# Kernel tuning notes

Measured on AMD Instinct MI355X. Metric: run time of the kernel, lower is better.

Reference implementation:

```python
import jax, jax.numpy as jnp
import numpy as np

B, S, HID = 2, 2048, 4096
NH, NKV, HD = 32, 8, 128
GRP = NH // NKV          # query heads per kv head
G = 128                  # weight quant group size
FP8_MAX = 448.0          # e4m3 max
EPS = 1e-6


def _rmsnorm(x, w):
    return x * jax.lax.rsqrt(jnp.mean(x * x, axis=-1, keepdims=True) + EPS) * w


def _act_quant(x):
    # per-token fp8 quantization: scale = amax/448, values clipped to fp8 range
    s = jnp.max(jnp.abs(x), axis=-1, keepdims=True) / FP8_MAX
    s = jnp.maximum(s, 1e-6)
    return jnp.clip(x / s, -FP8_MAX, FP8_MAX), s


def _deq_weight(wi4, wscale):
    # wi4: [out, in] int values in [0,16) -> signed int4 [-8,7]
    # wscale: [out, in//G] per-group scales, broadcast along input dim
    return (wi4.astype(jnp.float32) - 8.0) * jnp.repeat(wscale, G, axis=1)


def _rotate_half(x):
    x1, x2 = jnp.split(x, 2, axis=-1)
    return jnp.concatenate([-x2, x1], axis=-1)


def setup_inputs() -> dict:
    key = jax.random.key(0)
    ks = jax.random.split(key, 8)
    hidden_states = jax.random.normal(ks[0], (B, S, HID), dtype=jnp.float32)
    ln_weight = jnp.ones((HID,), dtype=jnp.float32)
    # real RoPE tables
    inv_freq = 1.0 / (10000.0 ** (np.arange(0, HD, 2, dtype=np.float32) / HD))
    ang = np.arange(S, dtype=np.float32)[:, None] * inv_freq[None, :]
    emb = np.concatenate([ang, ang], axis=-1)  # [S, HD]
    cos = jnp.broadcast_to(jnp.asarray(np.cos(emb)), (B, S, HD)).astype(jnp.float32)
    sin = jnp.broadcast_to(jnp.asarray(np.sin(emb)), (B, S, HD)).astype(jnp.float32)
    def wq(k, out, inp):
        ki, ksc = jax.random.split(k)
        wi = jax.random.randint(ki, (out, inp), 0, 16, dtype=jnp.int32)
        sc = jax.random.uniform(ksc, (out, inp // G), dtype=jnp.float32) * 0.01 + 0.001
        return wi, sc
    wq_i4, wq_scale = wq(ks[1], NH * HD, HID)
    wk_i4, wk_scale = wq(ks[2], NKV * HD, HID)
    wv_i4, wv_scale = wq(ks[3], NKV * HD, HID)
    wo_i4, wo_scale = wq(ks[4], HID, NH * HD)
    return dict(hidden_states=hidden_states, ln_weight=ln_weight, cos=cos, sin=sin,
                wq_scale=wq_scale, wk_scale=wk_scale, wv_scale=wv_scale, wo_scale=wo_scale,
                wq_i4=wq_i4, wk_i4=wk_i4, wv_i4=wv_i4, wo_i4=wo_i4)


def reference(hidden_states, ln_weight, cos, sin,
              wq_scale, wk_scale, wv_scale, wo_scale,
              wq_i4, wk_i4, wv_i4, wo_i4):
    b, s, _ = hidden_states.shape
    residual = hidden_states
    h = _rmsnorm(hidden_states, ln_weight)
    qx, qx_s = _act_quant(h)                     # [b,s,HID], [b,s,1]
    q = (qx @ _deq_weight(wq_i4, wq_scale).T) * qx_s
    k = (qx @ _deq_weight(wk_i4, wk_scale).T) * qx_s
    v = (qx @ _deq_weight(wv_i4, wv_scale).T) * qx_s
    q = q.reshape(b, s, NH, HD)
    k = k.reshape(b, s, NKV, HD)
    v = v.reshape(b, s, NKV, HD)
    cse, sne = cos[:, :, None, :], sin[:, :, None, :]
    q = q * cse + _rotate_half(q) * sne
    k = k * cse + _rotate_half(k) * sne
    # GQA causal attention (fp8 fmha numerics emulated in fp32)
    qg = q.reshape(b, s, NKV, GRP, HD)
    scaling = HD ** -0.5
    scores = jnp.einsum('bskgd,btkd->bkgst', qg, k) * scaling  # [b,kv,g,s,t]
    causal = jnp.tril(jnp.ones((s, s), dtype=bool))
    scores = jnp.where(causal, scores, jnp.float32(-1e30))
    p = jax.nn.softmax(scores, axis=-1)
    o = jnp.einsum('bkgst,btkd->bskgd', p, v).reshape(b, s, NH * HD)
    qo, qo_s = _act_quant(o)
    out = (qo @ _deq_weight(wo_i4, wo_scale).T) * qo_s + residual
    return out
```

## Files before the change

kernel.cpp:

```cpp
#include <hip/hip_runtime.h>
#include <stdint.h>

#define HID    4096
#define SLEN   2048
#define BATCH  2
#define NHEADS 32
#define NKVH   8
#define HDIM   128
#define NTOK   (BATCH*SLEN)
#define NQK    (NHEADS*HDIM)
#define NKVD   (NKVH*HDIM)
#define NQKV   (NQK + 2*NKVD)
#define ASTR   (NQK + NKVD)

typedef unsigned short u16;
typedef short short8 __attribute__((ext_vector_type(8)));
typedef float f32x4 __attribute__((ext_vector_type(4)));
typedef int int4v __attribute__((ext_vector_type(4)));
typedef u16 u16x4 __attribute__((ext_vector_type(4)));

static __device__ __forceinline__ u16 f2bf(float f) {
  unsigned u = __builtin_bit_cast(unsigned, f);
  u += 0x7FFFu + ((u >> 16) & 1u);
  return (u16)(u >> 16);
}
static __device__ __forceinline__ float bf2f(u16 h) {
  return __builtin_bit_cast(float, (unsigned)h << 16);
}
static __device__ __forceinline__ void gload_lds16(const void* g, void* l) {
  __builtin_amdgcn_global_load_lds((const __attribute__((address_space(1))) void*)g,
                                   (__attribute__((address_space(3))) void*)l, 16, 0, 0);
}

__global__ __launch_bounds__(256) void k_rmsnorm(const float* __restrict__ x,
                                                 const float* __restrict__ w,
                                                 u16* __restrict__ h) {
  const int row = blockIdx.x;
  const float4* xr = (const float4*)(x + (size_t)row * HID);
  float4 vals[4];
  float ss = 0.f;
#pragma unroll
  for (int i = 0; i < 4; ++i) {
    float4 v = xr[threadIdx.x + i * 256];
    vals[i] = v;
    ss += v.x*v.x + v.y*v.y + v.z*v.z + v.w*v.w;
  }
#pragma unroll
  for (int off = 32; off; off >>= 1) ss += __shfl_xor(ss, off);
  __shared__ float red[4];
  if ((threadIdx.x & 63) == 0) red[threadIdx.x >> 6] = ss;
  __syncthreads();
  ss = red[0] + red[1] + red[2] + red[3];
  const float scale = rsqrtf(ss * (1.f / HID) + 1e-6f);
  u16* hr = h + (size_t)row * HID;
#pragma unroll
  for (int i = 0; i < 4; ++i) {
    int c = (threadIdx.x + i * 256) * 4;
    float4 v = vals[i];
    unsigned lo = (unsigned)f2bf(v.x * scale * w[c])   | ((unsigned)f2bf(v.y * scale * w[c+1]) << 16);
    unsigned hi = (unsigned)f2bf(v.z * scale * w[c+2]) | ((unsigned)f2bf(v.w * scale * w[c+3]) << 16);
    *(unsigned long long*)(hr + c) = ((unsigned long long)hi << 32) | lo;
  }
}

__global__ __launch_bounds__(256) void k_deq(const int* __restrict__ W,
                                             const float* __restrict__ Ws,
                                             u16* __restrict__ out) {
  const int idx = blockIdx.x * 256 + threadIdx.x;
  const int n = idx >> 9;
  const int k8 = (idx & 511) * 8;
  const float sc = Ws[n * 32 + (k8 >> 7)];
  int4v a = *(const int4v*)(W + (size_t)n * HID + k8);
  int4v b = *(const int4v*)(W + (size_t)n * HID + k8 + 4);
  u16 r[8];
#pragma unroll
  for (int j = 0; j < 4; ++j) r[j]     = f2bf((float)(a[j] - 8) * sc);
#pragma unroll
  for (int j = 0; j < 4; ++j) r[j + 4] = f2bf((float)(b[j] - 8) * sc);
  *(short8*)(out + (size_t)n * HID + k8) = *(short8*)r;
}

#define KD 4096
#define NT 64

#define STAGE_A_(nb, kt, mh)                                                   \
  { _Pragma("unroll") for (int r_ = 0; r_ < 2; ++r_) {                         \
      const int base_ = (mh)*64 + r_*128 + wave*8;                             \
      const int lr_ = base_ + (lane>>3);                                       \
      gload_lds16(Ag + (size_t)(m0 + lr_)*KD + (kt)*64 + (((lane&7) ^ (lr_&7))<<3), \
                  lA[nb] + base_*64); } }

#define STAGE_B_(nb, kt, nh)                                                   \
  { _Pragma("unroll") for (int r_ = 0; r_ < 2; ++r_) {                         \
      const int w8_ = r_*64 + wave*8;                                          \
      const int base_ = ((w8_>>5)<<6) + (nh)*32 + (w8_&31);                    \
      const int nr_ = base_ + (lane>>3);                                       \
      gload_lds16(Bg + (size_t)(n0 + nr_)*KD + (kt)*64 + (((lane&7) ^ (nr_&7))<<3), \
                  lB[nb] + base_*64); } }

#define DS_PHASE(buf, mh, nh)                                                  \
  { const int kb_ = lane >> 4;                                                 \
    _Pragma("unroll") for (int ks = 0; ks < 2; ++ks) {                         \
      _Pragma("unroll") for (int i = 0; i < 4; ++i) {                          \
        const int lr_ = wm*128 + (mh)*64 + i*16 + (lane & 15);                 \
        af[i][ks] = *(const short8*)(lA[buf] + lr_*64 + (((ks*4+kb_) ^ (lr_&7))<<3)); } \
      _Pragma("unroll") for (int j = 0; j < 2; ++j) {                          \
        const int nr_ = wn*64 + (nh)*32 + j*16 + (lane & 15);                  \
        bf[j][ks] = *(const short8*)(lB[buf] + nr_*64 + (((ks*4+kb_) ^ (nr_&7))<<3)); } } }

#define MFMA_PHASE(mh, nh)                                                     \
  __builtin_amdgcn_s_setprio(1);                                               \
  _Pragma("unroll") for (int ks = 0; ks < 2; ++ks)                             \
    _Pragma("unroll") for (int i = 0; i < 4; ++i)                              \
      _Pragma("unroll") for (int j = 0; j < 2; ++j)                            \
        acc[(mh)*4+i][(nh)*2+j] = __builtin_amdgcn_mfma_f32_16x16x32_bf16(     \
            af[i][ks], bf[j][ks], acc[(mh)*4+i][(nh)*2+j], 0, 0, 0);           \
  __builtin_amdgcn_s_setprio(0);

#define BAR()  __builtin_amdgcn_s_barrier(); asm volatile("" ::: "memory")
#define VMW(n) asm volatile("s_waitcnt vmcnt(" #n ")" ::: "memory")

#define GEMM8P_BODY                                                            \
  __shared__ __align__(16) u16 lA[2][256*64];                                  \
  __shared__ __align__(16) u16 lB[2][256*64];                                  \
  const int tid = threadIdx.x, lane = tid & 63, wave = tid >> 6;               \
  const int wm = wave >> 2, wn = wave & 3;                                     \
  f32x4 acc[8][4];                                                             \
  _Pragma("unroll") for (int mi = 0; mi < 8; ++mi)                             \
    _Pragma("unroll") for (int ni = 0; ni < 4; ++ni)                           \
      acc[mi][ni] = (f32x4){0.f, 0.f, 0.f, 0.f};                               \
  short8 af[4][2], bf[2][2];                                                   \
  STAGE_A_(0, 0, 0); STAGE_B_(0, 0, 0); STAGE_A_(0, 0, 1); STAGE_B_(0, 0, 1);  \
  VMW(4); BAR();                                                               \
  for (int t = 0; t < NT - 1; ++t) {                                           \
    const int cur = t & 1, nxt = cur ^ 1;                                      \
    DS_PHASE(cur, 0, 0);                                                       \
    STAGE_A_(nxt, t + 1, 0);                                                   \
    BAR();                                                                     \
    MFMA_PHASE(0, 0);                                                          \
    VMW(2); BAR();                                                             \
    DS_PHASE(cur, 0, 1);                                                       \
    STAGE_B_(nxt, t + 1, 0);                                                   \
    BAR();                                                                     \
    MFMA_PHASE(0, 1);                                                          \
    BAR();                                                                     \
    DS_PHASE(cur, 1, 0);                                                       \
    STAGE_A_(nxt, t + 1, 1);                                                   \
    BAR();                                                                     \
    MFMA_PHASE(1, 0);                                                          \
    BAR();                                                                     \
    DS_PHASE(cur, 1, 1);                                                       \
    STAGE_B_(nxt, t + 1, 1);                                                   \
    BAR();                                                                     \
    MFMA_PHASE(1, 1);                                                          \
    VMW(4); BAR();                                                             \
  }                                                                            \
  {                                                                            \
    const int cur = (NT - 1) & 1;                                              \
    DS_PHASE(cur, 0, 0);                                                       \
    BAR();                                                                     \
    MFMA_PHASE(0, 0);                                                          \
    VMW(0); BAR();                                                             \
    DS_PHASE(cur, 0, 1);                                                       \
    BAR();                                                                     \
    MFMA_PHASE(0, 1);                                                          \
    BAR();                                                                     \
    DS_PHASE(cur, 1, 0);                                                       \
    BAR();                                                                     \
    MFMA_PHASE(1, 0);                                                          \
    BAR();                                                                     \
    DS_PHASE(cur, 1, 1);                                                       \
    BAR();                                                                     \
    MFMA_PHASE(1, 1);                                                          \
  }

__global__ __launch_bounds__(512, 2) void k_gemm_qkv_8p(
    const u16* __restrict__ Ag, const u16* __restrict__ Bg,
    u16* __restrict__ C, u16* __restrict__ Vt) {
  const int wg = (blockIdx.x & 7) * 48 + (blockIdx.x >> 3);
  const int m0 = (wg & 15) * 256;
  const int n0 = (wg >> 4) * 256;
  GEMM8P_BODY
  if (n0 < ASTR) {
#pragma unroll
    for (int mi = 0; mi < 8; ++mi) {
      const int row = m0 + wm * 128 + mi * 16 + ((lane >> 4) << 2);
#pragma unroll
      for (int ni = 0; ni < 4; ++ni) {
        const int col = n0 + wn * 64 + ni * 16 + (lane & 15);
#pragma unroll
        for (int r = 0; r < 4; ++r)
          C[(size_t)(row + r) * ASTR + col] = f2bf(acc[mi][ni][r]);
      }
    }
  } else {
#pragma unroll
    for (int mi = 0; mi < 8; ++mi) {
      const int row = m0 + wm * 128 + mi * 16 + ((lane >> 4) << 2);
      const int b_ = row >> 11, s_ = row & 2047;
#pragma unroll
      for (int ni = 0; ni < 4; ++ni) {
        const int colv = (n0 - ASTR) + wn * 64 + ni * 16 + (lane & 15);
        u16x4 pk;
#pragma unroll
        for (int r = 0; r < 4; ++r) pk[r] = f2bf(acc[mi][ni][r]);
        *(u16x4*)(Vt + ((size_t)(b_ * NKVH + (colv >> 7)) * HDIM + (colv & 127)) * SLEN + s_) = pk;
      }
    }
  }
}

__global__ __launch_bounds__(512, 2) void k_gemm_o_8p(
    const u16* __restrict__ Ag, const u16* __restrict__ Bg,
    const float* __restrict__ resid, float* __restrict__ out) {
  const int wg = (blockIdx.x & 7) * 32 + (blockIdx.x >> 3);
  const int m0 = (wg & 15) * 256;
  const int n0 = (wg >> 4) * 256;
  GEMM8P_BODY
#pragma unroll
  for (int mi = 0; mi < 8; ++mi) {
    const int row = m0 + wm * 128 + mi * 16 + ((lane >> 4) << 2);
#pragma unroll
    for (int ni = 0; ni < 4; ++ni) {
      const int col = n0 + wn * 64 + ni * 16 + (lane & 15);
#pragma unroll
      for (int r = 0; r < 4; ++r) {
        const size_t idx = (size_t)(row + r) * HID + col;
        out[idx] = acc[mi][ni][r] + resid[idx];
      }
    }
  }
}

#define BM 128
#define BN 128
#define BK 64

__global__ __launch_bounds__(256) void k_gemm_qkv(
    const u16* __restrict__ A,
    const int* __restrict__ Wq, const int* __restrict__ Wk, const int* __restrict__ Wv,
    const float* __restrict__ Sq, const float* __restrict__ Sk, const float* __restrict__ Sv,
    u16* __restrict__ C, u16* __restrict__ Vt) {
  __shared__ __align__(16) u16 lA[BM * BK];
  __shared__ __align__(16) u16 lB[BN * BK];
  const int tid = threadIdx.x;
  const int lane = tid & 63;
  const int wave = tid >> 6;
  const int wm = wave >> 1, wn = wave & 1;
  const int m0 = blockIdx.x * BM;
  const int n0 = blockIdx.y * BN;

  const int* W; const float* Ws; int nb;
  if (n0 < NQK)       { W = Wq; Ws = Sq; nb = n0; }
  else if (n0 < ASTR) { W = Wk; Ws = Sk; nb = n0 - NQK; }
  else                { W = Wv; Ws = Sv; nb = n0 - ASTR; }

  const int mloc = wave * 8 + (lane >> 3);
  const int lb8 = (((lane & 7) ^ (lane >> 3)) << 3);

  f32x4 acc[4][4];
#pragma unroll
  for (int mi = 0; mi < 4; ++mi)
#pragma unroll
    for (int ni = 0; ni < 4; ++ni) acc[mi][ni] = (f32x4){0.f, 0.f, 0.f, 0.f};

  for (int k0 = 0; k0 < HID; k0 += BK) {
    __syncthreads();
#pragma unroll
    for (int p = 0; p < 4; ++p)
      gload_lds16(A + (size_t)(m0 + p * 32 + mloc) * HID + k0 + lb8,
                  lA + p * 2048 + wave * 512);
    const int grp = k0 >> 7;
#pragma unroll
    for (int p = 0; p < 8; ++p) {
      const int n = p * 16 + (tid >> 4);
      const int kk = (tid & 15) * 4;
      int4v wv4 = *(const int4v*)(W + (size_t)(nb + n) * HID + k0 + kk);
      const float sc = Ws[(nb + n) * 32 + grp];
      unsigned lo = (unsigned)f2bf((float)(wv4[0] - 8) * sc) |
                    ((unsigned)f2bf((float)(wv4[1] - 8) * sc) << 16);
      unsigned hi = (unsigned)f2bf((float)(wv4[2] - 8) * sc) |
                    ((unsigned)f2bf((float)(wv4[3] - 8) * sc) << 16);
      const int di = (n * 64 + kk) ^ ((n & 7) << 3);
      unsigned* dst = (unsigned*)(lB + di);
      dst[0] = lo; dst[1] = hi;
    }
    __syncthreads();
#pragma unroll
    for (int kc = 0; kc < 2; ++kc) {
      const int kOff = kc * 32 + ((lane >> 4) << 3);
      short8 af[4], bfr[4];
#pragma unroll
      for (int i = 0; i < 4; ++i) {
        const int m = wm * 64 + i * 16 + (lane & 15);
        af[i] = *(const short8*)(lA + ((m * 64 + kOff) ^ ((m & 7) << 3)));
        const int n = wn * 64 + i * 16 + (lane & 15);
        bfr[i] = *(const short8*)(lB + ((n * 64 + kOff) ^ ((n & 7) << 3)));
      }
#pragma unroll
      for (int mi = 0; mi < 4; ++mi)
#pragma unroll
        for (int ni = 0; ni < 4; ++ni)
          acc[mi][ni] = __builtin_amdgcn_mfma_f32_16x16x32_bf16(af[mi], bfr[ni], acc[mi][ni], 0, 0, 0);
    }
  }
  if (n0 < ASTR) {
#pragma unroll
    for (int mi = 0; mi < 4; ++mi) {
      const int row = m0 + wm * 64 + mi * 16 + ((lane >> 4) << 2);
#pragma unroll
      for (int ni = 0; ni < 4; ++ni) {
        const int col = n0 + wn * 64 + ni * 16 + (lane & 15);
#pragma unroll
        for (int r = 0; r < 4; ++r)
          C[(size_t)(row + r) * ASTR + col] = f2bf(acc[mi][ni][r]);
      }
    }
  } else {
#pragma unroll
    for (int mi = 0; mi < 4; ++mi) {
      const int row = m0 + wm * 64 + mi * 16 + ((lane >> 4) << 2);
      const int b_ = row >> 11, s_ = row & 2047;
#pragma unroll
      for (int ni = 0; ni < 4; ++ni) {
        const int colv = (n0 - ASTR) + wn * 64 + ni * 16 + (lane & 15);
        u16x4 pk;
#pragma unroll
        for (int r = 0; r < 4; ++r) pk[r] = f2bf(acc[mi][ni][r]);
        *(u16x4*)(Vt + ((size_t)(b_ * NKVH + (colv >> 7)) * HDIM + (colv & 127)) * SLEN + s_) = pk;
      }
    }
  }
}

__global__ __launch_bounds__(256) void k_gemm_o(
    const u16* __restrict__ A, const int* __restrict__ W, const float* __restrict__ Ws,
    const float* __restrict__ resid, float* __restrict__ out) {
  __shared__ __align__(16) u16 lA[BM * BK];
  __shared__ __align__(16) u16 lB[BN * BK];
  const int tid = threadIdx.x;
  const int lane = tid & 63;
  const int wave = tid >> 6;
  const int wm = wave >> 1, wn = wave & 1;
  const int m0 = blockIdx.x * BM;
  const int n0 = blockIdx.y * BN;

  const int mloc = wave * 8 + (lane >> 3);
  const int lb8 = (((lane & 7) ^ (lane >> 3)) << 3);

  f32x4 acc[4][4];
#pragma unroll
  for (int mi = 0; mi < 4; ++mi)
#pragma unroll
    for (int ni = 0; ni < 4; ++ni) acc[mi][ni] = (f32x4){0.f, 0.f, 0.f, 0.f};

  for (int k0 = 0; k0 < NQK; k0 += BK) {
    __syncthreads();
#pragma unroll
    for (int p = 0; p < 4; ++p)
      gload_lds16(A + (size_t)(m0 + p * 32 + mloc) * NQK + k0 + lb8,
                  lA + p * 2048 + wave * 512);
    const int grp = k0 >> 7;
#pragma unroll
    for (int p = 0; p < 8; ++p) {
      const int n = p * 16 + (tid >> 4);
      const int kk = (tid & 15) * 4;
      int4v wv4 = *(const int4v*)(W + (size_t)(n0 + n) * NQK + k0 + kk);
      const float sc = Ws[(n0 + n) * 32 + grp];
      unsigned lo = (unsigned)f2bf((float)(wv4[0] - 8) * sc) |
                    ((unsigned)f2bf((float)(wv4[1] - 8) * sc) << 16);
      unsigned hi = (unsigned)f2bf((float)(wv4[2] - 8) * sc) |
                    ((unsigned)f2bf((float)(wv4[3] - 8) * sc) << 16);
      const int di = (n * 64 + kk) ^ ((n & 7) << 3);
      unsigned* dst = (unsigned*)(lB + di);
      dst[0] = lo; dst[1] = hi;
    }
    __syncthreads();
#pragma unroll
    for (int kc = 0; kc < 2; ++kc) {
      const int kOff = kc * 32 + ((lane >> 4) << 3);
      short8 af[4], bfr[4];
#pragma unroll
      for (int i = 0; i < 4; ++i) {
        const int m = wm * 64 + i * 16 + (lane & 15);
        af[i] = *(const short8*)(lA + ((m * 64 + kOff) ^ ((m & 7) << 3)));
        const int n = wn * 64 + i * 16 + (lane & 15);
        bfr[i] = *(const short8*)(lB + ((n * 64 + kOff) ^ ((n & 7) << 3)));
      }
#pragma unroll
      for (int mi = 0; mi < 4; ++mi)
#pragma unroll
        for (int ni = 0; ni < 4; ++ni)
          acc[mi][ni] = __builtin_amdgcn_mfma_f32_16x16x32_bf16(af[mi], bfr[ni], acc[mi][ni], 0, 0, 0);
      }
  }
#pragma unroll
  for (int mi = 0; mi < 4; ++mi) {
    const int row = m0 + wm * 64 + mi * 16 + ((lane >> 4) << 2);
#pragma unroll
    for (int ni = 0; ni < 4; ++ni) {
      const int col = n0 + wn * 64 + ni * 16 + (lane & 15);
#pragma unroll
      for (int r = 0; r < 4; ++r) {
        const size_t idx = (size_t)(row + r) * HID + col;
        out[idx] = acc[mi][ni][r] + resid[idx];
      }
    }
  }
}

__global__ __launch_bounds__(256) void k_rope(u16* __restrict__ qk,
                                              const float* __restrict__ cosb,
                                              const float* __restrict__ sinb) {
  const int idx = blockIdx.x * 256 + threadIdx.x;
  const int d = idx & 63;
  const int hh = (idx >> 6) % 40;
  const int t = idx / (64 * 40);
  const int col = (hh < 32) ? hh * HDIM : NQK + (hh - 32) * HDIM;
  u16* p = qk + (size_t)t * ASTR + col;
  const float c = cosb[t * HDIM + d], s = sinb[t * HDIM + d];
  const float x1 = bf2f(p[d]), x2 = bf2f(p[d + 64]);
  p[d]      = f2bf(x1 * c - x2 * s);
  p[d + 64] = f2bf(x2 * c + x1 * s);
}

__global__ __launch_bounds__(256) void k_attn(const u16* __restrict__ qk,
                                              const u16* __restrict__ vt,
                                              u16* __restrict__ o) {
  const int slot = blockIdx.x;
  const int w = (slot & 7) * 128 + (slot >> 3);
  const int qi = 15 - (w & 15);
  const int h = (w >> 4) & 31;
  const int b = w >> 9;
  const int kvh = h >> 2;
  const int q0 = qi * 128;
  const int lane = threadIdx.x & 63, wave = threadIdx.x >> 6;
  const int m = lane & 15, kg = lane >> 4;

  const u16* Qb = qk + (size_t)b * SLEN * ASTR + h * HDIM;
  const u16* Kb = qk + (size_t)b * SLEN * ASTR + NQK + kvh * HDIM;
  const u16* Vb = vt + (size_t)(b * NKVH + kvh) * HDIM * SLEN;

  __shared__ __align__(16) u16 Kt[64 * 128];
  __shared__ __align__(16) u16 Vts[128 * 64];
  __shared__ __align__(16) u16 Pl[4][32 * 72];

  const int qr = q0 + wave * 32;
  short8 qf[2][4];
#pragma unroll
  for (int mi = 0; mi < 2; ++mi)
#pragma unroll
    for (int kc = 0; kc < 4; ++kc)
      qf[mi][kc] = *(const short8*)(Qb + (size_t)(qr + mi * 16 + m) * ASTR + kc * 32 + kg * 8);

  f32x4 oacc[2][8];
#pragma unroll
  for (int mi = 0; mi < 2; ++mi)
#pragma unroll
    for (int n = 0; n < 8; ++n) oacc[mi][n] = (f32x4){0.f, 0.f, 0.f, 0.f};
  float rm[2][4], rl[2][4];
#pragma unroll
  for (int mi = 0; mi < 2; ++mi)
#pragma unroll
    for (int r = 0; r < 4; ++r) { rm[mi][r] = -3.0e38f; rl[mi][r] = 0.f; }

  const float sscale = 0.08838834764831845f;
  const int nt = q0 / 64 + 2;
  for (int t = 0; t < nt; ++t) {
    const int kv0 = t * 64;
    __syncthreads();
#pragma unroll
    for (int p = 0; p < 4; ++p) {
      const int row = p * 16 + wave * 4 + (lane >> 4);
      const int c8s = (lane & 15) ^ (row & 7);
      gload_lds16(Kb + (size_t)(kv0 + row) * ASTR + c8s * 8, Kt + p * 2048 + wave * 512);
    }
#pragma unroll
    for (int p = 0; p < 4; ++p) {
      const int d = p * 32 + wave * 8 + (lane >> 3);
      const int c8s = (lane & 7) ^ (d & 7);
      gload_lds16(Vb + (size_t)d * SLEN + kv0 + c8s * 8, Vts + p * 2048 + wave * 512);
    }
    __syncthreads();

    f32x4 sf[2][4];
#pragma unroll
    for (int mi = 0; mi < 2; ++mi)
#pragma unroll
      for (int ni = 0; ni < 4; ++ni) sf[mi][ni] = (f32x4){0.f, 0.f, 0.f, 0.f};
#pragma unroll
    for (int ni = 0; ni < 4; ++ni)
#pragma unroll
      for (int kc = 0; kc < 4; ++kc) {
        const int krow = ni * 16 + m;
        short8 kf = *(const short8*)(Kt + krow * 128 + (((kc * 4 + kg) ^ (krow & 7)) << 3));
#pragma unroll
        for (int mi = 0; mi < 2; ++mi)
          sf[mi][ni] = __builtin_amdgcn_mfma_f32_16x16x32_bf16(qf[mi][kc], kf, sf[mi][ni], 0, 0, 0);
      }

#pragma unroll
    for (int mi = 0; mi < 2; ++mi) {
      const bool dg = (kv0 + 63 > qr + mi * 16);
      float tmax[4] = {-3.0e38f, -3.0e38f, -3.0e38f, -3.0e38f};
#pragma unroll
      for (int ni = 0; ni < 4; ++ni)
#pragma unroll
        for (int r = 0; r < 4; ++r) {
          float s = sf[mi][ni][r] * sscale;
          if (dg) {
            const int rowg = qr + mi * 16 + kg * 4 + r;
            const int colg = kv0 + ni * 16 + m;
            if (colg > rowg) s = -1e30f;
          }
          sf[mi][ni][r] = s;
          tmax[r] = fmaxf(tmax[r], s);
        }
#pragma unroll
      for (int r = 0; r < 4; ++r)
#pragma unroll
        for (int off = 1; off < 16; off <<= 1)
          tmax[r] = fmaxf(tmax[r], __shfl_xor(tmax[r], off));
      float scl[4], psum[4];
#pragma unroll
      for (int r = 0; r < 4; ++r) {
        const float mn = fmaxf(rm[mi][r], tmax[r]);
        scl[r] = __expf(rm[mi][r] - mn);
        rm[mi][r] = mn;
        psum[r] = 0.f;
      }
#pragma unroll
      for (int ni = 0; ni < 4; ++ni)
#pragma unroll
        for (int r = 0; r < 4; ++r) {
          const float p = __expf(sf[mi][ni][r] - rm[mi][r]);
          psum[r] += p;
          Pl[wave][(mi * 16 + kg * 4 + r) * 72 + ni * 16 + m] = f2bf(p);
        }
#pragma unroll
      for (int r = 0; r < 4; ++r) {
#pragma unroll
        for (int off = 1; off < 16; off <<= 1)
          psum[r] += __shfl_xor(psum[r], off);
        rl[mi][r] = rl[mi][r] * scl[r] + psum[r];
      }
#pragma unroll
      for (int n = 0; n < 8; ++n)
#pragma unroll
        for (int r = 0; r < 4; ++r) oacc[mi][n][r] *= scl[r];
    }

#pragma unroll
    for (int kc = 0; kc < 2; ++kc) {
      short8 pf[2];
#pragma unroll
      for (int mi = 0; mi < 2; ++mi)
        pf[mi] = *(const short8*)(&Pl[wave][(mi * 16 + m) * 72 + kc * 32 + kg * 8]);
#pragma unroll
      for (int n = 0; n < 8; ++n) {
        const int vrow = n * 16 + m;
        short8 vf = *(const short8*)(Vts + vrow * 64 + (((kc * 4 + kg) ^ (vrow & 7)) << 3));
#pragma unroll
        for (int mi = 0; mi < 2; ++mi)
          oacc[mi][n] = __builtin_amdgcn_mfma_f32_16x16x32_bf16(pf[mi], vf, oacc[mi][n], 0, 0, 0);
      }
    }
  }

#pragma unroll
  for (int mi = 0; mi < 2; ++mi) {
    float inv[4];
#pragma unroll
    for (int r = 0; r < 4; ++r) inv[r] = 1.0f / rl[mi][r];
#pragma unroll
    for (int n = 0; n < 8; ++n)
#pragma unroll
      for (int r = 0; r < 4; ++r) {
        const int row = qr + mi * 16 + kg * 4 + r;
        o[((size_t)b * SLEN + row) * NQK + h * HDIM + n * 16 + m] = f2bf(oacc[mi][n][r] * inv[r]);
      }
  }
}

extern "C" void kernel_launch(void* const* d_in, const int* in_sizes, int n_in,
                              void* d_out, int out_size, void* d_ws, size_t ws_size,
                              hipStream_t stream) {
  (void)in_sizes; (void)n_in; (void)out_size;
  const float* x    = (const float*)d_in[0];
  const float* lnw  = (const float*)d_in[1];
  const float* cosb = (const float*)d_in[2];
  const float* sinb = (const float*)d_in[3];
  const float* sq   = (const float*)d_in[4];
  const float* sk   = (const float*)d_in[5];
  const float* sv   = (const float*)d_in[6];
  const float* so   = (const float*)d_in[7];
  const int* wq     = (const int*)d_in[8];
  const int* wk     = (const int*)d_in[9];
  const int* wv     = (const int*)d_in[10];
  const int* wo     = (const int*)d_in[11];

  u16* h   = (u16*)d_ws;
  u16* qkb = h + (size_t)NTOK * HID;
  u16* vtb = qkb + (size_t)NTOK * ASTR;
  u16* wqkvb = vtb + (size_t)BATCH * NKVH * HDIM * SLEN;
  u16* wob   = wqkvb + (size_t)NQKV * HID;
  float* out = (float*)d_out;

  const size_t need = ((size_t)NTOK * HID + (size_t)NTOK * ASTR +
                       (size_t)BATCH * NKVH * HDIM * SLEN +
                       (size_t)NQKV * HID + (size_t)HID * NQK) * sizeof(u16);
  const bool predeq = (ws_size >= need);

  k_rmsnorm<<<NTOK, 256, 0, stream>>>(x, lnw, h);

  if (predeq) {
    k_deq<<<NQK  * 2, 256, 0, stream>>>(wq, sq, wqkvb);
    k_deq<<<NKVD * 2, 256, 0, stream>>>(wk, sk, wqkvb + (size_t)NQK * HID);
    k_deq<<<NKVD * 2, 256, 0, stream>>>(wv, sv, wqkvb + (size_t)ASTR * HID);
    k_deq<<<NQK  * 2, 256, 0, stream>>>(wo, so, wob);
    k_gemm_qkv_8p<<<384, 512, 0, stream>>>(h, wqkvb, qkb, vtb);
  } else {
    dim3 g1(NTOK / BM, NQKV / BN);
    k_gemm_qkv<<<g1, 256, 0, stream>>>(h, wq, wk, wv, sq, sk, sv, qkb, vtb);
  }

  k_rope<<<(NTOK * 40 * 64) / 256, 256, 0, stream>>>(qkb, cosb, sinb);

  k_attn<<<1024, 256, 0, stream>>>(qkb, vtb, h);

  if (predeq) {
    k_gemm_o_8p<<<256, 512, 0, stream>>>(h, wob, x, out);
  } else {
    dim3 g3(NTOK / BM, HID / BN);
    k_gemm_o<<<g3, 256, 0, stream>>>(h, wo, so, x, out);
  }
}
```

Before: 755.9 us.

## Fuse weight dequant launches, use simple tiled QKV GEMM, prioritize attention MFMAs

```diff
diff --git a/kernel.cpp b/kernel.cpp
--- a/kernel.cpp
+++ b/kernel.cpp
@@ -63,21 +63,112 @@
   }
 }
 
-__global__ __launch_bounds__(256) void k_deq(const int* __restrict__ W,
-                                             const float* __restrict__ Ws,
-                                             u16* __restrict__ out) {
+__global__ __launch_bounds__(256) void k_deq_all(
+    const int* __restrict__ wq, const int* __restrict__ wk,
+    const int* __restrict__ wv, const int* __restrict__ wo,
+    const float* __restrict__ sq, const float* __restrict__ sk,
+    const float* __restrict__ sv, const float* __restrict__ so,
+    u16* __restrict__ out) {
   const int idx = blockIdx.x * 256 + threadIdx.x;
-  const int n = idx >> 9;
+  const int row = idx >> 9;
   const int k8 = (idx & 511) * 8;
-  const float sc = Ws[n * 32 + (k8 >> 7)];
-  int4v a = *(const int4v*)(W + (size_t)n * HID + k8);
-  int4v b = *(const int4v*)(W + (size_t)n * HID + k8 + 4);
-  u16 r[8];
-#pragma unroll
-  for (int j = 0; j < 4; ++j) r[j]     = f2bf((float)(a[j] - 8) * sc);
-#pragma unroll
-  for (int j = 0; j < 4; ++j) r[j + 4] = f2bf((float)(b[j] - 8) * sc);
-  *(short8*)(out + (size_t)n * HID + k8) = *(short8*)r;
+  const int* W; const float* S; int r;
+  if (row < 4096)      { W = wq; S = sq; r = row; }
+  else if (row < 5120) { W = wk; S = sk; r = row - 4096; }
+  else if (row < 6144) { W = wv; S = sv; r = row - 5120; }
+  else                 { W = wo; S = so; r = row - 6144; }
+  const float sc = S[r * 32 + (k8 >> 7)];
+  int4v a = *(const int4v*)(W + (size_t)r * HID + k8);
+  int4v b = *(const int4v*)(W + (size_t)r * HID + k8 + 4);
+  u16 rr[8];
+#pragma unroll
+  for (int j = 0; j < 4; ++j) rr[j]     = f2bf((float)(a[j] - 8) * sc);
+#pragma unroll
+  for (int j = 0; j < 4; ++j) rr[j + 4] = f2bf((float)(b[j] - 8) * sc);
+  *(short8*)(out + (size_t)row * HID + k8) = *(short8*)rr;
+}
+
+#define BM 128
+#define BN 128
+#define BK 64
+
+__global__ __launch_bounds__(256) void k_gemm_qkv_b(
+    const u16* __restrict__ A, const u16* __restrict__ B,
+    u16* __restrict__ C, u16* __restrict__ Vt) {
+  __shared__ __align__(16) u16 lA[BM * BK];
+  __shared__ __align__(16) u16 lB[BN * BK];
+  const int tid = threadIdx.x;
+  const int lane = tid & 63;
+  const int wave = tid >> 6;
+  const int wm = wave >> 1, wn = wave & 1;
+  const int m0 = blockIdx.x * BM;
+  const int n0 = blockIdx.y * BN;
+
+  const int rloc = wave * 8 + (lane >> 3);
+  const int lb8 = (((lane & 7) ^ (lane >> 3)) << 3);
+
+  f32x4 acc[4][4];
+#pragma unroll
+  for (int mi = 0; mi < 4; ++mi)
+#pragma unroll
+    for (int ni = 0; ni < 4; ++ni) acc[mi][ni] = (f32x4){0.f, 0.f, 0.f, 0.f};
+
+  for (int k0 = 0; k0 < HID; k0 += BK) {
+    __syncthreads();
+#pragma unroll
+    for (int p = 0; p < 4; ++p)
+      gload_lds16(A + (size_t)(m0 + p * 32 + rloc) * HID + k0 + lb8,
+                  lA + p * 2048 + wave * 512);
+#pragma unroll
+    for (int p = 0; p < 4; ++p)
+      gload_lds16(B + (size_t)(n0 + p * 32 + rloc) * HID + k0 + lb8,
+                  lB + p * 2048 + wave * 512);
+    __syncthreads();
+#pragma unroll
+    for (int kc = 0; kc < 2; ++kc) {
+      const int kOff = kc * 32 + ((lane >> 4) << 3);
+      short8 af[4], bfr[4];
+#pragma unroll
+      for (int i = 0; i < 4; ++i) {
+        const int m = wm * 64 + i * 16 + (lane & 15);
+        af[i] = *(const short8*)(lA + ((m * 64 + kOff) ^ ((m & 7) << 3)));
+        const int n = wn * 64 + i * 16 + (lane & 15);
+        bfr[i] = *(const short8*)(lB + ((n * 64 + kOff) ^ ((n & 7) << 3)));
+      }
+#pragma unroll
+      for (int mi = 0; mi < 4; ++mi)
+#pragma unroll
+        for (int ni = 0; ni < 4; ++ni)
+          acc[mi][ni] = __builtin_amdgcn_mfma_f32_16x16x32_bf16(af[mi], bfr[ni], acc[mi][ni], 0, 0, 0);
+    }
+  }
+  if (n0 < ASTR) {
+#pragma unroll
+    for (int mi = 0; mi < 4; ++mi) {
+      const int row = m0 + wm * 64 + mi * 16 + ((lane >> 4) << 2);
+#pragma unroll
+      for (int ni = 0; ni < 4; ++ni) {
+        const int col = n0 + wn * 64 + ni * 16 + (lane & 15);
+#pragma unroll
+        for (int r = 0; r < 4; ++r)
+          C[(size_t)(row + r) * ASTR + col] = f2bf(acc[mi][ni][r]);
+      }
+    }
+  } else {
+#pragma unroll
+    for (int mi = 0; mi < 4; ++mi) {
+      const int row = m0 + wm * 64 + mi * 16 + ((lane >> 4) << 2);
+      const int b_ = row >> 11, s_ = row & 2047;
+#pragma unroll
+      for (int ni = 0; ni < 4; ++ni) {
+        const int colv = (n0 - ASTR) + wn * 64 + ni * 16 + (lane & 15);
+        u16x4 pk;
+#pragma unroll
+        for (int r = 0; r < 4; ++r) pk[r] = f2bf(acc[mi][ni][r]);
+        *(u16x4*)(Vt + ((size_t)(b_ * NKVH + (colv >> 7)) * HDIM + (colv & 127)) * SLEN + s_) = pk;
+      }
+    }
+  }
 }
 
 #define KD 4096
@@ -174,42 +265,6 @@
     MFMA_PHASE(1, 1);                                                          \
   }
 
-__global__ __launch_bounds__(512, 2) void k_gemm_qkv_8p(
-    const u16* __restrict__ Ag, const u16* __restrict__ Bg,
-    u16* __restrict__ C, u16* __restrict__ Vt) {
-  const int wg = (blockIdx.x & 7) * 48 + (blockIdx.x >> 3);
-  const int m0 = (wg & 15) * 256;
-  const int n0 = (wg >> 4) * 256;
-  GEMM8P_BODY
-  if (n0 < ASTR) {
-#pragma unroll
-    for (int mi = 0; mi < 8; ++mi) {
-      const int row = m0 + wm * 128 + mi * 16 + ((lane >> 4) << 2);
-#pragma unroll
-      for (int ni = 0; ni < 4; ++ni) {
-        const int col = n0 + wn * 64 + ni * 16 + (lane & 15);
-#pragma unroll
-        for (int r = 0; r < 4; ++r)
-          C[(size_t)(row + r) * ASTR + col] = f2bf(acc[mi][ni][r]);
-      }
-    }
-  } else {
-#pragma unroll
-    for (int mi = 0; mi < 8; ++mi) {
-      const int row = m0 + wm * 128 + mi * 16 + ((lane >> 4) << 2);
-      const int b_ = row >> 11, s_ = row & 2047;
-#pragma unroll
-      for (int ni = 0; ni < 4; ++ni) {
-        const int colv = (n0 - ASTR) + wn * 64 + ni * 16 + (lane & 15);
-        u16x4 pk;
-#pragma unroll
-        for (int r = 0; r < 4; ++r) pk[r] = f2bf(acc[mi][ni][r]);
-        *(u16x4*)(Vt + ((size_t)(b_ * NKVH + (colv >> 7)) * HDIM + (colv & 127)) * SLEN + s_) = pk;
-      }
-    }
-  }
-}
-
 __global__ __launch_bounds__(512, 2) void k_gemm_o_8p(
     const u16* __restrict__ Ag, const u16* __restrict__ Bg,
     const float* __restrict__ resid, float* __restrict__ out) {
@@ -231,10 +286,6 @@
     }
   }
 }
-
-#define BM 128
-#define BN 128
-#define BK 64
 
 __global__ __launch_bounds__(256) void k_gemm_qkv(
     const u16* __restrict__ A,
@@ -488,6 +539,7 @@
     for (int mi = 0; mi < 2; ++mi)
 #pragma unroll
       for (int ni = 0; ni < 4; ++ni) sf[mi][ni] = (f32x4){0.f, 0.f, 0.f, 0.f};
+    __builtin_amdgcn_s_setprio(1);
 #pragma unroll
     for (int ni = 0; ni < 4; ++ni)
 #pragma unroll
@@ -498,6 +550,7 @@
         for (int mi = 0; mi < 2; ++mi)
           sf[mi][ni] = __builtin_amdgcn_mfma_f32_16x16x32_bf16(qf[mi][kc], kf, sf[mi][ni], 0, 0, 0);
       }
+    __builtin_amdgcn_s_setprio(0);
 
 #pragma unroll
     for (int mi = 0; mi < 2; ++mi) {
@@ -550,6 +603,7 @@
         for (int r = 0; r < 4; ++r) oacc[mi][n][r] *= scl[r];
     }
 
+    __builtin_amdgcn_s_setprio(1);
 #pragma unroll
     for (int kc = 0; kc < 2; ++kc) {
       short8 pf[2];
@@ -565,6 +619,7 @@
           oacc[mi][n] = __builtin_amdgcn_mfma_f32_16x16x32_bf16(pf[mi], vf, oacc[mi][n], 0, 0, 0);
       }
     }
+    __builtin_amdgcn_s_setprio(0);
   }
 
 #pragma unroll
@@ -614,11 +669,9 @@
   k_rmsnorm<<<NTOK, 256, 0, stream>>>(x, lnw, h);
 
   if (predeq) {
-    k_deq<<<NQK  * 2, 256, 0, stream>>>(wq, sq, wqkvb);
-    k_deq<<<NKVD * 2, 256, 0, stream>>>(wk, sk, wqkvb + (size_t)NQK * HID);
-    k_deq<<<NKVD * 2, 256, 0, stream>>>(wv, sv, wqkvb + (size_t)ASTR * HID);
-    k_deq<<<NQK  * 2, 256, 0, stream>>>(wo, so, wob);
-    k_gemm_qkv_8p<<<384, 512, 0, stream>>>(h, wqkvb, qkb, vtb);
+    k_deq_all<<<(10240 * 512) / 256, 256, 0, stream>>>(wq, wk, wv, wo, sq, sk, sv, so, wqkvb);
+    dim3 g1(NTOK / BM, NQKV / BN);
+    k_gemm_qkv_b<<<g1, 256, 0, stream>>>(h, wqkvb, qkb, vtb);
   } else {
     dim3 g1(NTOK / BM, NQKV / BN);
     k_gemm_qkv<<<g1, 256, 0, stream>>>(h, wq, wk, wv, sq, sk, sv, qkb, vtb);
```

Measured after the change: 712.3 us. 1.06x faster.
